# Kernel tuning notes

Measured on AMD Instinct MI355X. Metric: run time of the kernel, lower is better.

## Reference

```python
import jax, jax.numpy as jnp
import numpy as np

WS = 7
HEADS = 8
DIM = 256
IN_DIM = 128
HID = 1024
EPS = 1e-5


def _rel_index(ws):
    coords = np.stack(np.meshgrid(np.arange(ws), np.arange(ws), indexing='ij'))  # (2,ws,ws)
    cf = coords.reshape(2, -1)                      # (2,N)
    rel = (cf[:, :, None] - cf[:, None, :]).transpose(1, 2, 0).copy()  # (N,N,2)
    rel[..., 0] += ws - 1
    rel[..., 1] += ws - 1
    rel[..., 0] *= 2 * ws - 1
    return rel.sum(-1)  # (N,N) int

REL_IDX = jnp.asarray(_rel_index(WS).reshape(-1))


def layernorm(x, g, b):
    mu = jnp.mean(x, axis=-1, keepdims=True)
    var = jnp.mean(jnp.square(x - mu), axis=-1, keepdims=True)
    return (x - mu) * jax.lax.rsqrt(var + EPS) * g + b


def setup_inputs() -> dict:
    key = jax.random.key(0)
    ks = jax.random.split(key, 16)
    s = 0.02
    return {
        'x': jax.random.normal(ks[0], (16, IN_DIM, 56, 56), jnp.float32),
        'conv_w': jax.random.normal(ks[1], (DIM, IN_DIM, 3, 3), jnp.float32) * s,
        'conv_b': jnp.zeros((DIM,), jnp.float32),
        'g1': jnp.ones((DIM,), jnp.float32), 'b1': jnp.zeros((DIM,), jnp.float32),
        'g2': jnp.ones((DIM,), jnp.float32), 'b2': jnp.zeros((DIM,), jnp.float32),
        'g3': jnp.ones((DIM,), jnp.float32), 'b3': jnp.zeros((DIM,), jnp.float32),
        'qkv_w': jax.random.normal(ks[2], (3 * DIM, DIM), jnp.float32) * s,
        'rel_bias_table': jax.random.normal(ks[3], ((2 * WS - 1) ** 2, HEADS), jnp.float32) * s,
        'proj_w': jax.random.normal(ks[4], (DIM, DIM), jnp.float32) * s,
        'proj_b': jnp.zeros((DIM,), jnp.float32),
        'fc1_w': jax.random.normal(ks[5], (HID, DIM), jnp.float32) * s,
        'fc1_b': jnp.zeros((HID,), jnp.float32),
        'fc2_w': jax.random.normal(ks[6], (DIM, HID), jnp.float32) * s,
        'fc2_b': jnp.zeros((DIM,), jnp.float32),
    }


def reference(x, conv_w, conv_b, g1, b1, g2, b2, g3, b3, qkv_w, rel_bias_table,
              proj_w, proj_b, fc1_w, fc1_b, fc2_w, fc2_b):
    # proj_q: 3x3 conv, stride 1, pad 1 (input_dim != embed_dim)
    x = jax.lax.conv_general_dilated(
        x, conv_w, window_strides=(1, 1), padding=((1, 1), (1, 1)),
        dimension_numbers=('NCHW', 'OIHW', 'NCHW')) + conv_b[None, :, None, None]
    b, c, h, w = x.shape
    x = x.reshape(b, c, h * w).transpose(0, 2, 1)  # (b, n, c)
    x = layernorm(x, g1, b1)
    x = x.reshape(b, h, w, c)
    pb = (WS - h % WS) % WS
    pr = (WS - w % WS) % WS
    x = jnp.pad(x, ((0, 0), (0, pb), (0, pr), (0, 0)))
    hp, wp = h + pb, w + pr
    # window partition -> (nW, N, c)
    xw = x.reshape(b, hp // WS, WS, wp // WS, WS, c)
    xw = xw.transpose(0, 1, 3, 2, 4, 5).reshape(-1, WS * WS, c)
    nW, N, _ = xw.shape
    d = c // HEADS
    qkv = (xw @ qkv_w.T).reshape(nW, N, 3, HEADS, d).transpose(2, 0, 3, 1, 4)  # (3,nW,h,N,d)
    q, k, v = qkv[0] * (d ** -0.5), qkv[1], qkv[2]
    attn = jnp.einsum('whnd,whmd->whnm', q, k)
    bias = rel_bias_table[REL_IDX].reshape(N, N, HEADS).transpose(2, 0, 1)  # (h,N,N)
    attn = jax.nn.softmax(attn + bias[None], axis=-1)
    out = jnp.einsum('whnm,whmd->whnd', attn, v).transpose(0, 2, 1, 3).reshape(nW, N, c)
    out = out @ proj_w.T + proj_b
    # window reverse
    x = out.reshape(b, hp // WS, wp // WS, WS, WS, c)
    x = x.transpose(0, 1, 3, 2, 4, 5).reshape(b, hp, wp, c)
    x = x[:, :h, :w, :].reshape(b, h * w, c)
    # NOTE: faithful to source — NO residual from pre-attention stream
    x = layernorm(x, g2, b2)
    x = jax.nn.gelu(x @ fc1_w.T + fc1_b, approximate=False) @ fc2_w.T + fc2_b
    x = x + x  # source: x = x + drop_path(x) with identity drop_path
    x = layernorm(x, g3, b3)
    return x.reshape(b, h, w, c).transpose(0, 3, 1, 2)
```

## Files before the change

### kernel.cpp

```cpp
#include <hip/hip_runtime.h>
#include <hip/hip_bf16.h>

typedef unsigned short u16;
typedef unsigned int   u32;

#define TTOK  50176
#define CDIM  256

using short8 = __attribute__((ext_vector_type(8))) short;
using f32x4  = __attribute__((ext_vector_type(4))) float;

__device__ __forceinline__ float b2f(u16 u) { return __uint_as_float(((u32)u) << 16); }
__device__ __forceinline__ u16 f2b(float f) {
    u32 x = __float_as_uint(f);
    return (u16)((x + 0x7fffu + ((x >> 16) & 1u)) >> 16);
}

#define GLD16(src, dst) __builtin_amdgcn_global_load_lds( \
    (const __attribute__((address_space(1))) void*)(src),  \
    (__attribute__((address_space(3))) void*)(dst), 16, 0, 0)

__global__ __launch_bounds__(256) void cvt4_k(const float* __restrict__ a, const float* __restrict__ b,
                                              const float* __restrict__ c, const float* __restrict__ d,
                                              u16* __restrict__ dst) {
    int i = blockIdx.x * 256 + threadIdx.x;
    const float* src; int off;
    if (i < 49152)       { src = a; off = i; }
    else if (i < 65536)  { src = b; off = i - 49152; }
    else if (i < 131072) { src = c; off = i - 65536; }
    else                 { src = d; off = i - 131072; }
    float4 v = *(const float4*)&src[off * 4];
    ushort4 o;
    o.x = f2b(v.x); o.y = f2b(v.y); o.z = f2b(v.z); o.w = f2b(v.w);
    *(ushort4*)&dst[i * 4] = o;
}

__global__ __launch_bounds__(256) void pad_k(const float* __restrict__ x, u16* __restrict__ xp) {
    __shared__ float tile[128][58];
    int bid = blockIdx.x;
    int b = bid / 58, hp = bid - b * 58;
    int tid = threadIdx.x;
    bool zrow = (hp == 0 || hp == 57);
    if (!zrow) {
        int h = hp - 1;
        for (int e = tid; e < 128 * 14; e += 256) {
            int ic = e / 14, j = e - ic * 14;
            float4 v = *(const float4*)&x[(((size_t)b * 128 + ic) * 56 + h) * 56 + j * 4];
            tile[ic][j * 4 + 0] = v.x; tile[ic][j * 4 + 1] = v.y;
            tile[ic][j * 4 + 2] = v.z; tile[ic][j * 4 + 3] = v.w;
        }
        __syncthreads();
    }
    size_t rb = ((size_t)b * 58 + hp) * 58 * 128;
    for (int u = tid; u < 58 * 16; u += 256) {
        int wp = u / 16, icg = u - wp * 16;
        uint4 o = make_uint4(0u, 0u, 0u, 0u);
        if (!zrow && wp != 0 && wp != 57) {
            int w = wp - 1, ic0 = icg * 8;
            u16 v0 = f2b(tile[ic0 + 0][w]), v1 = f2b(tile[ic0 + 1][w]);
            u16 v2 = f2b(tile[ic0 + 2][w]), v3 = f2b(tile[ic0 + 3][w]);
            u16 v4 = f2b(tile[ic0 + 4][w]), v5 = f2b(tile[ic0 + 5][w]);
            u16 v6 = f2b(tile[ic0 + 6][w]), v7 = f2b(tile[ic0 + 7][w]);
            o.x = (u32)v0 | ((u32)v1 << 16);
            o.y = (u32)v2 | ((u32)v3 << 16);
            o.z = (u32)v4 | ((u32)v5 << 16);
            o.w = (u32)v6 | ((u32)v7 << 16);
        }
        *(uint4*)&xp[rb + (size_t)wp * 128 + icg * 8] = o;
    }
}

__global__ __launch_bounds__(256) void w2_k(const float* __restrict__ w, u16* __restrict__ o2) {
    int e = blockIdx.x * 256 + threadIdx.x;
    int o = e / 1152, rem = e - o * 1152;
    int tap = rem >> 7, ic = rem & 127;
    o2[e] = f2b(w[(o * 128 + ic) * 9 + tap]);
}

__device__ __forceinline__ void xcd_remap(int& bx, int& by) {
    int nx = gridDim.x, ny = gridDim.y;
    if ((ny & 7) == 0) {
        int linear = blockIdx.y * nx + blockIdx.x;
        int xcd = linear & 7, within = linear >> 3;
        bx = within % nx;
        by = xcd * (ny >> 3) + within / nx;
    } else { bx = blockIdx.x; by = blockIdx.y; }
}

__device__ __forceinline__ int xcd_remap1d() {
    int nb = gridDim.x, lin = blockIdx.x;
    int q = nb >> 3, r = nb & 7;
    int xcd = lin & 7, idx = lin >> 3;
    return (xcd < r ? xcd * (q + 1) : r * (q + 1) + (xcd - r) * q) + idx;
}

__global__ __launch_bounds__(256) void gemm_conv_ln_k(const u16* __restrict__ xp, const u16* __restrict__ W2,
                                                      const float* __restrict__ bias,
                                                      const float* __restrict__ gam, const float* __restrict__ bet,
                                                      u16* __restrict__ C) {
    __shared__ __align__(16) u16 lsA[64 * 64];
    __shared__ __align__(16) u16 lsB[256 * 64];
    int tid = threadIdx.x;
    int wave = tid >> 6, lane = tid & 63;
    int by = xcd_remap1d();
    int mBase = by * 64;
    int wm = wave >> 1, wn = wave & 1;
    int lr = lane & 15, lq = lane >> 4;
    int r8 = lane >> 3, kg = lane & 7;
    int kgsw = ((kg ^ r8) & 7) * 8;

    size_t tb[2]; const u16* gB[8];
#pragma unroll
    for (int j = 0; j < 2; ++j) {
        int t = mBase + wave * 16 + j * 8 + r8;
        int win = t / 49, n = t - win * 49;
        int b = win >> 6, wh = (win >> 3) & 7, ww = win & 7;
        int r = n / 7, s = n - r * 7;
        tb[j] = ((size_t)(b * 58 + wh * 7 + r) * 58 + ww * 7 + s) * 128 + kgsw;
    }
#pragma unroll
    for (int j = 0; j < 8; ++j)
        gB[j] = W2 + (size_t)(wave * 64 + j * 8 + r8) * 1152 + kgsw;

    f32x4 acc[2][8];
#pragma unroll
    for (int m = 0; m < 2; ++m)
#pragma unroll
        for (int n = 0; n < 8; ++n) acc[m][n] = (f32x4){0.f, 0.f, 0.f, 0.f};

    for (int ks = 0; ks < 18; ++ks) {
        int tap = ks >> 1, half = ks & 1;
        int kh = tap / 3, kw = tap - kh * 3;
        int uoff = (kh * 58 + kw) * 128 + half * 64;
#pragma unroll
        for (int j = 0; j < 2; ++j) GLD16(xp + tb[j] + uoff, lsA + (wave * 16 + j * 8) * 64);
#pragma unroll
        for (int j = 0; j < 8; ++j) GLD16(gB[j] + ks * 64, lsB + (wave * 64 + j * 8) * 64);
        __syncthreads();
#pragma unroll
        for (int kk = 0; kk < 2; ++kk) {
            int sl = (((kk << 2) | lq) ^ (lr & 7)) * 8;
            short8 af[2], bf[8];
#pragma unroll
            for (int m = 0; m < 2; ++m)
                af[m] = *(const short8*)&lsA[(wm * 32 + m * 16 + lr) * 64 + sl];
#pragma unroll
            for (int n = 0; n < 8; ++n)
                bf[n] = *(const short8*)&lsB[(wn * 128 + n * 16 + lr) * 64 + sl];
#pragma unroll
            for (int m = 0; m < 2; ++m)
#pragma unroll
                for (int n = 0; n < 8; ++n)
                    acc[m][n] = __builtin_amdgcn_mfma_f32_16x16x32_bf16(af[m], bf[n], acc[m][n], 0, 0, 0);
        }
        __syncthreads();
    }

    float bv[8], gv[8], btv[8];
#pragma unroll
    for (int n = 0; n < 8; ++n) {
        int col = wn * 128 + n * 16 + lr;
        bv[n] = bias[col]; gv[n] = gam[col]; btv[n] = bet[col];
    }
#pragma unroll
    for (int m = 0; m < 2; ++m)
#pragma unroll
        for (int n = 0; n < 8; ++n)
#pragma unroll
            for (int r = 0; r < 4; ++r) acc[m][n][r] += bv[n];

    float* red = (float*)lsA;
#pragma unroll
    for (int m = 0; m < 2; ++m)
#pragma unroll
        for (int r = 0; r < 4; ++r) {
            float s = 0.f, qq = 0.f;
#pragma unroll
            for (int n = 0; n < 8; ++n) { float v = acc[m][n][r]; s += v; qq += v * v; }
            s += __shfl_xor(s, 1); s += __shfl_xor(s, 2); s += __shfl_xor(s, 4); s += __shfl_xor(s, 8);
            qq += __shfl_xor(qq, 1); qq += __shfl_xor(qq, 2); qq += __shfl_xor(qq, 4); qq += __shfl_xor(qq, 8);
            if (lr == 0) {
                int row = wm * 32 + m * 16 + lq * 4 + r;
                red[row * 4 + wn * 2] = s; red[row * 4 + wn * 2 + 1] = qq;
            }
        }
    __syncthreads();

#pragma unroll
    for (int m = 0; m < 2; ++m)
#pragma unroll
        for (int r = 0; r < 4; ++r) {
            int row = wm * 32 + m * 16 + lq * 4 + r;
            float S = red[row * 4] + red[row * 4 + 2];
            float Q = red[row * 4 + 1] + red[row * 4 + 3];
            float mean = S * (1.f / 256.f);
            float var = Q * (1.f / 256.f) - mean * mean;
            float inv = rsqrtf(var + 1e-5f);
            size_t grow = (size_t)(mBase + row) * 256;
#pragma unroll
            for (int n = 0; n < 8; ++n) {
                int col = wn * 128 + n * 16 + lr;
                C[grow + col] = f2b((acc[m][n][r] - mean) * inv * gv[n] + btv[n]);
            }
        }
}

__global__ __launch_bounds__(256) void gemm_ln_k(const u16* __restrict__ A, const u16* __restrict__ Bw,
                                                 const float* __restrict__ bias,
                                                 const float* __restrict__ gam, const float* __restrict__ bet,
                                                 u16* __restrict__ C, int K) {
    __shared__ __align__(16) u16 lsA[64 * 64];
    __shared__ __align__(16) u16 lsB[256 * 64];
    int tid = threadIdx.x;
    int wave = tid >> 6, lane = tid & 63;
    int by = xcd_remap1d();
    int mBase = by * 64;
    int wm = wave >> 1, wn = wave & 1;
    int lr = lane & 15, lq = lane >> 4;
    int r8 = lane >> 3, kg = lane & 7;
    int kgsw = ((kg ^ r8) & 7) * 8;

    const u16* gA[2]; const u16* gB[8];
#pragma unroll
    for (int j = 0; j < 2; ++j)
        gA[j] = A + (size_t)(mBase + wave * 16 + j * 8 + r8) * K + kgsw;
#pragma unroll
    for (int j = 0; j < 8; ++j)
        gB[j] = Bw + (size_t)(wave * 64 + j * 8 + r8) * K + kgsw;

    f32x4 acc[2][8];
#pragma unroll
    for (int m = 0; m < 2; ++m)
#pragma unroll
        for (int n = 0; n < 8; ++n) acc[m][n] = (f32x4){0.f, 0.f, 0.f, 0.f};

    for (int k0 = 0; k0 < K; k0 += 64) {
#pragma unroll
        for (int j = 0; j < 2; ++j) GLD16(gA[j] + k0, lsA + (wave * 16 + j * 8) * 64);
#pragma unroll
        for (int j = 0; j < 8; ++j) GLD16(gB[j] + k0, lsB + (wave * 64 + j * 8) * 64);
        __syncthreads();
#pragma unroll
        for (int kk = 0; kk < 2; ++kk) {
            int sl = (((kk << 2) | lq) ^ (lr & 7)) * 8;
            short8 af[2], bf[8];
#pragma unroll
            for (int m = 0; m < 2; ++m)
                af[m] = *(const short8*)&lsA[(wm * 32 + m * 16 + lr) * 64 + sl];
#pragma unroll
            for (int n = 0; n < 8; ++n)
                bf[n] = *(const short8*)&lsB[(wn * 128 + n * 16 + lr) * 64 + sl];
#pragma unroll
            for (int m = 0; m < 2; ++m)
#pragma unroll
                for (int n = 0; n < 8; ++n)
                    acc[m][n] = __builtin_amdgcn_mfma_f32_16x16x32_bf16(af[m], bf[n], acc[m][n], 0, 0, 0);
        }
        __syncthreads();
    }

    float bv[8], gv[8], btv[8];
#pragma unroll
    for (int n = 0; n < 8; ++n) {
        int col = wn * 128 + n * 16 + lr;
        bv[n] = bias[col]; gv[n] = gam[col]; btv[n] = bet[col];
    }
#pragma unroll
    for (int m = 0; m < 2; ++m)
#pragma unroll
        for (int n = 0; n < 8; ++n)
#pragma unroll
            for (int r = 0; r < 4; ++r) acc[m][n][r] += bv[n];

    float* red = (float*)lsA;
#pragma unroll
    for (int m = 0; m < 2; ++m)
#pragma unroll
        for (int r = 0; r < 4; ++r) {
            float s = 0.f, qq = 0.f;
#pragma unroll
            for (int n = 0; n < 8; ++n) { float v = acc[m][n][r]; s += v; qq += v * v; }
            s += __shfl_xor(s, 1); s += __shfl_xor(s, 2); s += __shfl_xor(s, 4); s += __shfl_xor(s, 8);
            qq += __shfl_xor(qq, 1); qq += __shfl_xor(qq, 2); qq += __shfl_xor(qq, 4); qq += __shfl_xor(qq, 8);
            if (lr == 0) {
                int row = wm * 32 + m * 16 + lq * 4 + r;
                red[row * 4 + wn * 2] = s; red[row * 4 + wn * 2 + 1] = qq;
            }
        }
    __syncthreads();

#pragma unroll
    for (int m = 0; m < 2; ++m)
#pragma unroll
        for (int r = 0; r < 4; ++r) {
            int row = wm * 32 + m * 16 + lq * 4 + r;
            float S = red[row * 4] + red[row * 4 + 2];
            float Q = red[row * 4 + 1] + red[row * 4 + 3];
            float mean = S * (1.f / 256.f);
            float var = Q * (1.f / 256.f) - mean * mean;
            float inv = rsqrtf(var + 1e-5f);
            size_t grow = (size_t)(mBase + row) * 256;
#pragma unroll
            for (int n = 0; n < 8; ++n) {
                int col = wn * 128 + n * 16 + lr;
                C[grow + col] = f2b((acc[m][n][r] - mean) * inv * gv[n] + btv[n]);
            }
        }
}

template <int EPI>
__global__ __launch_bounds__(256) void gemm_k(const u16* __restrict__ A, const u16* __restrict__ Bw,
                                              const float* __restrict__ bias, u16* __restrict__ C,
                                              int M, int N, int K) {
    __shared__ __align__(16) u16 lsA[2][128 * 32];
    __shared__ __align__(16) u16 lsB[2][128 * 32];
    int tid = threadIdx.x;
    int wave = tid >> 6, lane = tid & 63;
    int bx, by; xcd_remap(bx, by);
    int mBase = by * 128, nBase = bx * 128;
    int wm = wave >> 1, wn = wave & 1;
    int lr = lane & 15, lq = lane >> 4;
    int rr = lane >> 2, kc = lane & 3;
    int kcs = (kc ^ ((rr >> 1) & 3)) * 8;

    const u16* gA[2]; const u16* gB[2];
#pragma unroll
    for (int j = 0; j < 2; ++j) {
        int row = wave * 32 + j * 16 + rr;
        gA[j] = A  + (size_t)(mBase + row) * K + kcs;
        gB[j] = Bw + (size_t)(nBase + row) * K + kcs;
    }

    f32x4 acc[4][4];
#pragma unroll
    for (int m = 0; m < 4; ++m)
#pragma unroll
        for (int n = 0; n < 4; ++n) acc[m][n] = (f32x4){0.f, 0.f, 0.f, 0.f};

    int nk = K >> 5;
#pragma unroll
    for (int j = 0; j < 2; ++j) {
        GLD16(gA[j], &lsA[0][(wave * 32 + j * 16) * 32]);
        GLD16(gB[j], &lsB[0][(wave * 32 + j * 16) * 32]);
    }
    __syncthreads();

    int slq = (lq ^ ((lr >> 1) & 3)) * 8;
    for (int ks = 0; ks < nk; ++ks) {
        int cur = ks & 1;
        if (ks + 1 < nk) {
            int nxt = cur ^ 1;
            int ko = (ks + 1) << 5;
#pragma unroll
            for (int j = 0; j < 2; ++j) {
                GLD16(gA[j] + ko, &lsA[nxt][(wave * 32 + j * 16) * 32]);
                GLD16(gB[j] + ko, &lsB[nxt][(wave * 32 + j * 16) * 32]);
            }
        }
        short8 af[4], bf[4];
#pragma unroll
        for (int m = 0; m < 4; ++m)
            af[m] = *(const short8*)&lsA[cur][(wm * 64 + m * 16 + lr) * 32 + slq];
#pragma unroll
        for (int n = 0; n < 4; ++n)
            bf[n] = *(const short8*)&lsB[cur][(wn * 64 + n * 16 + lr) * 32 + slq];
#pragma unroll
        for (int m = 0; m < 4; ++m)
#pragma unroll
            for (int n = 0; n < 4; ++n)
                acc[m][n] = __builtin_amdgcn_mfma_f32_16x16x32_bf16(af[m], bf[n], acc[m][n], 0, 0, 0);
        __syncthreads();
    }

#pragma unroll
    for (int m = 0; m < 4; ++m) {
        int row0 = mBase + wm * 64 + m * 16 + lq * 4;
#pragma unroll
        for (int n = 0; n < 4; ++n) {
            int col = nBase + wn * 64 + n * 16 + lr;
            float bv = (EPI >= 1) ? bias[col] : 0.f;
#pragma unroll
            for (int r = 0; r < 4; ++r) {
                float v = acc[m][n][r] + bv;
                if (EPI == 2) {
                    float u = 0.79788456f * (v + 0.044715f * v * v * v);
                    float e = __expf(-2.f * u);
                    v = v * __frcp_rn(1.f + e);
                }
                C[(size_t)(row0 + r) * N + col] = f2b(v);
            }
        }
    }
}

__global__ __launch_bounds__(256) void attn_mfma_k(const u16* __restrict__ qkv,
                                                   const float* __restrict__ tab,
                                                   u16* __restrict__ out) {
    __shared__ __align__(16) u16 sh[28488];
    int tid = threadIdx.x;
    int wave = tid >> 6, lane = tid & 63;
    int wh = blockIdx.x * 4 + wave;
    int win = wh >> 3, head = wh & 7;
    int g = lane >> 4, cc = lane & 15;

    u16* Pl = sh + wave * 4608;
    u16* Vl = sh + 18432 + wave * 2176;
    float* bs = (float*)(sh + 27136) + wave * 169;

    const size_t wbase = (size_t)win * 49 * 768;
    for (int e = lane; e < 169; e += 64) bs[e] = tab[e * 8 + head];
    for (int e = lane; e < 49 * 16; e += 64) {
        int k = e >> 4, d0 = (e & 15) * 2;
        *(u32*)&Vl[k * 34 + d0] = *(const u32*)&qkv[wbase + (size_t)k * 768 + 512 + head * 32 + d0];
    }
    for (int e = lane; e < 15 * 16; e += 64) {
        int k = 49 + (e >> 4), d0 = (e & 15) * 2;
        *(u32*)&Vl[k * 34 + d0] = 0u;
    }
    __syncthreads();

    short8 aQ[4], bK[4];
#pragma unroll
    for (int t = 0; t < 4; ++t) {
        int qr = t * 16 + cc; if (qr > 48) qr = 48;
        aQ[t] = *(const short8*)&qkv[wbase + (size_t)qr * 768 + head * 32 + g * 8];
        int kr = t * 16 + cc; if (kr > 48) kr = 48;
        bK[t] = *(const short8*)&qkv[wbase + (size_t)kr * 768 + 256 + head * 32 + g * 8];
    }
    f32x4 S[4][4];
#pragma unroll
    for (int a = 0; a < 4; ++a)
#pragma unroll
        for (int b = 0; b < 4; ++b)
            S[a][b] = __builtin_amdgcn_mfma_f32_16x16x32_bf16(aQ[a], bK[b], (f32x4){0.f,0.f,0.f,0.f}, 0, 0, 0);

    int AqA[4][4];
#pragma unroll
    for (int tr = 0; tr < 4; ++tr)
#pragma unroll
        for (int r = 0; r < 4; ++r) {
            int q = tr * 16 + g * 4 + r; if (q > 48) q = 48;
            int dq = (q * 37) >> 8;
            AqA[tr][r] = 6 * dq + q + 84;
        }
    int AcA[4];
    bool colBad[4];
#pragma unroll
    for (int tc = 0; tc < 4; ++tc) {
        int c = tc * 16 + cc;
        colBad[tc] = (c > 48);
        if (c > 48) c = 48;
        int dc = (c * 37) >> 8;
        AcA[tc] = 6 * dc + c;
    }
    const float scale = 0.17677669529663687f;
    float inv[4][4];
#pragma unroll
    for (int tr = 0; tr < 4; ++tr) {
#pragma unroll
        for (int r = 0; r < 4; ++r) {
            float z0 = colBad[0] ? -1e30f : S[tr][0][r] * scale + bs[AqA[tr][r] - AcA[0]];
            float z1 = colBad[1] ? -1e30f : S[tr][1][r] * scale + bs[AqA[tr][r] - AcA[1]];
            float z2 = colBad[2] ? -1e30f : S[tr][2][r] * scale + bs[AqA[tr][r] - AcA[2]];
            float z3 = colBad[3] ? -1e30f : S[tr][3][r] * scale + bs[AqA[tr][r] - AcA[3]];
            float mx = fmaxf(fmaxf(z0, z1), fmaxf(z2, z3));
            mx = fmaxf(mx, __shfl_xor(mx, 1));
            mx = fmaxf(mx, __shfl_xor(mx, 2));
            mx = fmaxf(mx, __shfl_xor(mx, 4));
            mx = fmaxf(mx, __shfl_xor(mx, 8));
            float p0 = __expf(z0 - mx), p1 = __expf(z1 - mx);
            float p2 = __expf(z2 - mx), p3 = __expf(z3 - mx);
            S[tr][0][r] = p0; S[tr][1][r] = p1; S[tr][2][r] = p2; S[tr][3][r] = p3;
            float sm = p0 + p1 + p2 + p3;
            sm += __shfl_xor(sm, 1); sm += __shfl_xor(sm, 2);
            sm += __shfl_xor(sm, 4); sm += __shfl_xor(sm, 8);
            inv[tr][r] = 1.0f / sm;
        }
    }

#pragma unroll
    for (int tr = 0; tr < 4; ++tr)
#pragma unroll
        for (int tc = 0; tc < 4; ++tc) {
            int k = tc * 16 + cc;
            u16* pb = &Pl[tr * 1152 + k * 18 + g * 4];
            u32 w0 = (u32)f2b(S[tr][tc][0]) | ((u32)f2b(S[tr][tc][1]) << 16);
            u32 w1 = (u32)f2b(S[tr][tc][2]) | ((u32)f2b(S[tr][tc][3]) << 16);
            *(u32*)pb = w0;
            *(u32*)(pb + 2) = w1;
        }
    __syncthreads();

    f32x4 O[4][2];
#pragma unroll
    for (int a = 0; a < 4; ++a) { O[a][0] = (f32x4){0.f,0.f,0.f,0.f}; O[a][1] = (f32x4){0.f,0.f,0.f,0.f}; }
#pragma unroll
    for (int s = 0; s < 2; ++s) {
        short8 pa[4], vb[2];
#pragma unroll
        for (int tr = 0; tr < 4; ++tr)
#pragma unroll
            for (int j = 0; j < 8; ++j)
                pa[tr][j] = (short)Pl[tr * 1152 + (s * 32 + g * 8 + j) * 18 + cc];
#pragma unroll
        for (int td = 0; td < 2; ++td)
#pragma unroll
            for (int j = 0; j < 8; ++j)
                vb[td][j] = (short)Vl[(s * 32 + g * 8 + j) * 34 + td * 16 + cc];
#pragma unroll
        for (int tr = 0; tr < 4; ++tr)
#pragma unroll
            for (int td = 0; td < 2; ++td)
                O[tr][td] = __builtin_amdgcn_mfma_f32_16x16x32_bf16(pa[tr], vb[td], O[tr][td], 0, 0, 0);
    }

#pragma unroll
    for (int tr = 0; tr < 4; ++tr)
#pragma unroll
        for (int r = 0; r < 4; ++r) {
            int q = tr * 16 + g * 4 + r;
            if (q < 49) {
                float iv = inv[tr][r];
                u16* op = out + (size_t)(win * 49 + q) * 256 + head * 32;
                op[cc]      = f2b(O[tr][0][r] * iv);
                op[16 + cc] = f2b(O[tr][1][r] * iv);
            }
        }
}

__global__ __launch_bounds__(256) void ln3_out_k(const u16* __restrict__ f, const float* __restrict__ g3,
                                                 const float* __restrict__ b3, float* __restrict__ out) {
    __shared__ float tile[256][57];
    int bh = blockIdx.x;
    int b = bh / 56, h = bh - b * 56;
    int wv = threadIdx.x >> 6, lane = threadIdx.x & 63;
    int wh = h / 7, r = h - wh * 7;
    float4 gg = *(const float4*)&g3[lane * 4];
    float4 bb = *(const float4*)&b3[lane * 4];
    for (int i = 0; i < 14; ++i) {
        int w = wv + i * 4;
        int wwn = w / 7, s2 = w - wwn * 7;
        int t = (b * 64 + wh * 8 + wwn) * 49 + r * 7 + s2;
        ushort4 u = *(const ushort4*)&f[(size_t)t * 256 + lane * 4];
        float v0 = 2.f * b2f(u.x), v1 = 2.f * b2f(u.y), v2 = 2.f * b2f(u.z), v3 = 2.f * b2f(u.w);
        float s = v0 + v1 + v2 + v3;
        float q = v0 * v0 + v1 * v1 + v2 * v2 + v3 * v3;
#pragma unroll
        for (int o = 32; o; o >>= 1) { s += __shfl_xor(s, o); q += __shfl_xor(q, o); }
        float mean = s * (1.f / 256.f);
        float var = q * (1.f / 256.f) - mean * mean;
        float inv = rsqrtf(var + 1e-5f);
        int c = lane * 4;
        tile[c + 0][w] = (v0 - mean) * inv * gg.x + bb.x;
        tile[c + 1][w] = (v1 - mean) * inv * gg.y + bb.y;
        tile[c + 2][w] = (v2 - mean) * inv * gg.z + bb.z;
        tile[c + 3][w] = (v3 - mean) * inv * gg.w + bb.w;
    }
    __syncthreads();
    size_t obase = (size_t)b * 256 * 3136 + (size_t)h * 56;
#pragma unroll
    for (int it = 0; it < 28; ++it) {
        int e = it * 256 + threadIdx.x;
        int c = e / 28, wu = e - c * 28;
        float2 pack = make_float2(tile[c][wu * 2], tile[c][wu * 2 + 1]);
        *(float2*)&out[obase + (size_t)c * 3136 + wu * 2] = pack;
    }
}

extern "C" void kernel_launch(void* const* d_in, const int* in_sizes, int n_in,
                              void* d_out, int out_size, void* d_ws, size_t ws_size,
                              hipStream_t stream) {
    (void)in_sizes; (void)n_in; (void)out_size;
    const float* x      = (const float*)d_in[0];
    const float* conv_w = (const float*)d_in[1];
    const float* conv_b = (const float*)d_in[2];
    const float* g1     = (const float*)d_in[3];
    const float* b1     = (const float*)d_in[4];
    const float* g2     = (const float*)d_in[5];
    const float* b2     = (const float*)d_in[6];
    const float* g3     = (const float*)d_in[7];
    const float* b3     = (const float*)d_in[8];
    const float* qkv_w  = (const float*)d_in[9];
    const float* tab    = (const float*)d_in[10];
    const float* proj_w = (const float*)d_in[11];
    const float* proj_b = (const float*)d_in[12];
    const float* fc1_w  = (const float*)d_in[13];
    const float* fc1_b  = (const float*)d_in[14];
    const float* fc2_w  = (const float*)d_in[15];
    const float* fc2_b  = (const float*)d_in[16];
    float* outp = (float*)d_out;

    const size_t OFF_Y  = (size_t)TTOK * 1152 * 2;
    const size_t OFF_AT = OFF_Y + (size_t)TTOK * 512;
    const size_t NEED   = OFF_AT + (size_t)TTOK * 512;
    if (ws_size < NEED) return;

    char* ws = (char*)d_ws;
    u16* xpad    = (u16*)ws;
    u16* ybuf    = (u16*)(ws + OFF_Y);
    u16* atout   = (u16*)(ws + OFF_AT);
    u16* qkvbuf  = (u16*)ws;
    u16* hidden  = (u16*)ws;
    u16* W2      = atout;
    u16* wbase   = (u16*)(ws + (size_t)TTOK * 1024 * 2);
    u16* qkvw_b  = wbase;
    u16* projw_b = wbase + 196608;
    u16* fc1w_b  = projw_b + 65536;
    u16* fc2w_b  = fc1w_b + 262144;

    pad_k<<<928, 256, 0, stream>>>(x, xpad);
    w2_k<<<1152, 256, 0, stream>>>(conv_w, W2);
    cvt4_k<<<768, 256, 0, stream>>>(qkv_w, proj_w, fc1_w, fc2_w, qkvw_b);
    gemm_conv_ln_k<<<784, 256, 0, stream>>>(xpad, W2, conv_b, g1, b1, ybuf);
    gemm_k<0><<<dim3(6, 392), 256, 0, stream>>>(ybuf, qkvw_b, nullptr, qkvbuf, TTOK, 768, 256);
    attn_mfma_k<<<2048, 256, 0, stream>>>(qkvbuf, tab, atout);
    gemm_ln_k<<<784, 256, 0, stream>>>(atout, projw_b, proj_b, g2, b2, ybuf, 256);
    gemm_k<2><<<dim3(8, 392), 256, 0, stream>>>(ybuf, fc1w_b, fc1_b, hidden, TTOK, 1024, 256);
    gemm_k<1><<<dim3(2, 392), 256, 0, stream>>>(hidden, fc2w_b, fc2_b, atout, TTOK, 256, 1024);
    ln3_out_k<<<896, 256, 0, stream>>>(atout, g3, b3, outp);
}
```

Before: 326.1 us.

## Double-buffer LDS in conv/LN GEMMs and vectorize general GEMM epilogue stores

```diff
diff --git a/kernel.cpp b/kernel.cpp
--- a/kernel.cpp
+++ b/kernel.cpp
@@ -98,29 +98,29 @@
                                                       const float* __restrict__ bias,
                                                       const float* __restrict__ gam, const float* __restrict__ bet,
                                                       u16* __restrict__ C) {
-    __shared__ __align__(16) u16 lsA[64 * 64];
-    __shared__ __align__(16) u16 lsB[256 * 64];
+    __shared__ __align__(16) u16 lsA[2][64 * 32];
+    __shared__ __align__(16) u16 lsB[2][256 * 32];
     int tid = threadIdx.x;
     int wave = tid >> 6, lane = tid & 63;
     int by = xcd_remap1d();
     int mBase = by * 64;
     int wm = wave >> 1, wn = wave & 1;
     int lr = lane & 15, lq = lane >> 4;
-    int r8 = lane >> 3, kg = lane & 7;
-    int kgsw = ((kg ^ r8) & 7) * 8;
-
-    size_t tb[2]; const u16* gB[8];
-#pragma unroll
-    for (int j = 0; j < 2; ++j) {
-        int t = mBase + wave * 16 + j * 8 + r8;
+    int rr4 = lane >> 2, kc = lane & 3;
+    int kcs = (kc ^ ((rr4 >> 1) & 3)) * 8;
+
+    size_t tbA;
+    {
+        int t = mBase + wave * 16 + rr4;
         int win = t / 49, n = t - win * 49;
         int b = win >> 6, wh = (win >> 3) & 7, ww = win & 7;
         int r = n / 7, s = n - r * 7;
-        tb[j] = ((size_t)(b * 58 + wh * 7 + r) * 58 + ww * 7 + s) * 128 + kgsw;
-    }
-#pragma unroll
-    for (int j = 0; j < 8; ++j)
-        gB[j] = W2 + (size_t)(wave * 64 + j * 8 + r8) * 1152 + kgsw;
+        tbA = ((size_t)(b * 58 + wh * 7 + r) * 58 + ww * 7 + s) * 128 + kcs;
+    }
+    const u16* gB[4];
+#pragma unroll
+    for (int j = 0; j < 4; ++j)
+        gB[j] = W2 + (size_t)(j * 64 + wave * 16 + rr4) * 1152 + kcs;
 
     f32x4 acc[2][8];
 #pragma unroll
@@ -128,33 +128,36 @@
 #pragma unroll
         for (int n = 0; n < 8; ++n) acc[m][n] = (f32x4){0.f, 0.f, 0.f, 0.f};
 
-    for (int ks = 0; ks < 18; ++ks) {
-        int tap = ks >> 1, half = ks & 1;
-        int kh = tap / 3, kw = tap - kh * 3;
-        int uoff = (kh * 58 + kw) * 128 + half * 64;
-#pragma unroll
-        for (int j = 0; j < 2; ++j) GLD16(xp + tb[j] + uoff, lsA + (wave * 16 + j * 8) * 64);
-#pragma unroll
-        for (int j = 0; j < 8; ++j) GLD16(gB[j] + ks * 64, lsB + (wave * 64 + j * 8) * 64);
+#define CONV_STAGE(ks, buf) do { \
+        int tap_ = (ks) >> 2, qz_ = (ks) & 3; \
+        int kh_ = tap_ / 3, kw_ = tap_ - kh_ * 3; \
+        GLD16(xp + tbA + (kh_ * 58 + kw_) * 128 + qz_ * 32, &lsA[buf][(wave * 16 + rr4) * 32]); \
+        _Pragma("unroll") \
+        for (int j_ = 0; j_ < 4; ++j_) \
+            GLD16(gB[j_] + (ks) * 32, &lsB[buf][(j_ * 64 + wave * 16 + rr4) * 32]); \
+    } while (0)
+
+    CONV_STAGE(0, 0);
+    __syncthreads();
+    int slq = (lq ^ ((lr >> 1) & 3)) * 8;
+    for (int ks = 0; ks < 36; ++ks) {
+        int cur = ks & 1;
+        if (ks + 1 < 36) CONV_STAGE(ks + 1, cur ^ 1);
+        short8 af[2], bf[8];
+#pragma unroll
+        for (int m = 0; m < 2; ++m)
+            af[m] = *(const short8*)&lsA[cur][(wm * 32 + m * 16 + lr) * 32 + slq];
+#pragma unroll
+        for (int n = 0; n < 8; ++n)
+            bf[n] = *(const short8*)&lsB[cur][(wn * 128 + n * 16 + lr) * 32 + slq];
+#pragma unroll
+        for (int m = 0; m < 2; ++m)
+#pragma unroll
+            for (int n = 0; n < 8; ++n)
+                acc[m][n] = __builtin_amdgcn_mfma_f32_16x16x32_bf16(af[m], bf[n], acc[m][n], 0, 0, 0);
         __syncthreads();
-#pragma unroll
-        for (int kk = 0; kk < 2; ++kk) {
-            int sl = (((kk << 2) | lq) ^ (lr & 7)) * 8;
-            short8 af[2], bf[8];
-#pragma unroll
-            for (int m = 0; m < 2; ++m)
-                af[m] = *(const short8*)&lsA[(wm * 32 + m * 16 + lr) * 64 + sl];
-#pragma unroll
-            for (int n = 0; n < 8; ++n)
-                bf[n] = *(const short8*)&lsB[(wn * 128 + n * 16 + lr) * 64 + sl];
-#pragma unroll
-            for (int m = 0; m < 2; ++m)
-#pragma unroll
-                for (int n = 0; n < 8; ++n)
-                    acc[m][n] = __builtin_amdgcn_mfma_f32_16x16x32_bf16(af[m], bf[n], acc[m][n], 0, 0, 0);
-        }
-        __syncthreads();
-    }
+    }
+#undef CONV_STAGE
 
     float bv[8], gv[8], btv[8];
 #pragma unroll
@@ -209,24 +212,22 @@
                                                  const float* __restrict__ bias,
                                                  const float* __restrict__ gam, const float* __restrict__ bet,
                                                  u16* __restrict__ C, int K) {
-    __shared__ __align__(16) u16 lsA[64 * 64];
-    __shared__ __align__(16) u16 lsB[256 * 64];
+    __shared__ __align__(16) u16 lsA[2][64 * 32];
+    __shared__ __align__(16) u16 lsB[2][256 * 32];
     int tid = threadIdx.x;
     int wave = tid >> 6, lane = tid & 63;
     int by = xcd_remap1d();
     int mBase = by * 64;
     int wm = wave >> 1, wn = wave & 1;
     int lr = lane & 15, lq = lane >> 4;
-    int r8 = lane >> 3, kg = lane & 7;
-    int kgsw = ((kg ^ r8) & 7) * 8;
-
-    const u16* gA[2]; const u16* gB[8];
-#pragma unroll
-    for (int j = 0; j < 2; ++j)
-        gA[j] = A + (size_t)(mBase + wave * 16 + j * 8 + r8) * K + kgsw;
-#pragma unroll
-    for (int j = 0; j < 8; ++j)
-        gB[j] = Bw + (size_t)(wave * 64 + j * 8 + r8) * K + kgsw;
+    int rr4 = lane >> 2, kc = lane & 3;
+    int kcs = (kc ^ ((rr4 >> 1) & 3)) * 8;
+
+    const u16* gA = A + (size_t)(mBase + wave * 16 + rr4) * K + kcs;
+    const u16* gB[4];
+#pragma unroll
+    for (int j = 0; j < 4; ++j)
+        gB[j] = Bw + (size_t)(j * 64 + wave * 16 + rr4) * K + kcs;
 
     f32x4 acc[2][8];
 #pragma unroll
@@ -234,30 +235,35 @@
 #pragma unroll
         for (int n = 0; n < 8; ++n) acc[m][n] = (f32x4){0.f, 0.f, 0.f, 0.f};
 
-    for (int k0 = 0; k0 < K; k0 += 64) {
-#pragma unroll
-        for (int j = 0; j < 2; ++j) GLD16(gA[j] + k0, lsA + (wave * 16 + j * 8) * 64);
-#pragma unroll
-        for (int j = 0; j < 8; ++j) GLD16(gB[j] + k0, lsB + (wave * 64 + j * 8) * 64);
+#define LN_STAGE(ks, buf) do { \
+        GLD16(gA + (ks) * 32, &lsA[buf][(wave * 16 + rr4) * 32]); \
+        _Pragma("unroll") \
+        for (int j_ = 0; j_ < 4; ++j_) \
+            GLD16(gB[j_] + (ks) * 32, &lsB[buf][(j_ * 64 + wave * 16 + rr4) * 32]); \
+    } while (0)
+
+    int nk = K >> 5;
+    LN_STAGE(0, 0);
+    __syncthreads();
+    int slq = (lq ^ ((lr >> 1) & 3)) * 8;
+    for (int ks = 0; ks < nk; ++ks) {
+        int cur = ks & 1;
+        if (ks + 1 < nk) LN_STAGE(ks + 1, cur ^ 1);
+        short8 af[2], bf[8];
+#pragma unroll
+        for (int m = 0; m < 2; ++m)
+            af[m] = *(const short8*)&lsA[cur][(wm * 32 + m * 16 + lr) * 32 + slq];
+#pragma unroll
+        for (int n = 0; n < 8; ++n)
+            bf[n] = *(const short8*)&lsB[cur][(wn * 128 + n * 16 + lr) * 32 + slq];
+#pragma unroll
+        for (int m = 0; m < 2; ++m)
+#pragma unroll
+            for (int n = 0; n < 8; ++n)
+                acc[m][n] = __builtin_amdgcn_mfma_f32_16x16x32_bf16(af[m], bf[n], acc[m][n], 0, 0, 0);
         __syncthreads();
-#pragma unroll
-        for (int kk = 0; kk < 2; ++kk) {
-            int sl = (((kk << 2) | lq) ^ (lr & 7)) * 8;
-            short8 af[2], bf[8];
-#pragma unroll
-            for (int m = 0; m < 2; ++m)
-                af[m] = *(const short8*)&lsA[(wm * 32 + m * 16 + lr) * 64 + sl];
-#pragma unroll
-            for (int n = 0; n < 8; ++n)
-                bf[n] = *(const short8*)&lsB[(wn * 128 + n * 16 + lr) * 64 + sl];
-#pragma unroll
-            for (int m = 0; m < 2; ++m)
-#pragma unroll
-                for (int n = 0; n < 8; ++n)
-                    acc[m][n] = __builtin_amdgcn_mfma_f32_16x16x32_bf16(af[m], bf[n], acc[m][n], 0, 0, 0);
-        }
-        __syncthreads();
-    }
+    }
+#undef LN_STAGE
 
     float bv[8], gv[8], btv[8];
 #pragma unroll
@@ -368,27 +374,37 @@
         for (int m = 0; m < 4; ++m)
 #pragma unroll
             for (int n = 0; n < 4; ++n)
-                acc[m][n] = __builtin_amdgcn_mfma_f32_16x16x32_bf16(af[m], bf[n], acc[m][n], 0, 0, 0);
+                acc[m][n] = __builtin_amdgcn_mfma_f32_16x16x32_bf16(bf[n], af[m], acc[m][n], 0, 0, 0);
         __syncthreads();
     }
 
 #pragma unroll
     for (int m = 0; m < 4; ++m) {
-        int row0 = mBase + wm * 64 + m * 16 + lq * 4;
+        int row = mBase + wm * 64 + m * 16 + lr;
+        u16* crow = C + (size_t)row * N;
 #pragma unroll
         for (int n = 0; n < 4; ++n) {
-            int col = nBase + wn * 64 + n * 16 + lr;
-            float bv = (EPI >= 1) ? bias[col] : 0.f;
-#pragma unroll
-            for (int r = 0; r < 4; ++r) {
-                float v = acc[m][n][r] + bv;
-                if (EPI == 2) {
-                    float u = 0.79788456f * (v + 0.044715f * v * v * v);
-                    float e = __expf(-2.f * u);
-                    v = v * __frcp_rn(1.f + e);
-                }
-                C[(size_t)(row0 + r) * N + col] = f2b(v);
-            }
+            int col0 = nBase + wn * 64 + n * 16 + lq * 4;
+            float b0 = 0.f, b1 = 0.f, b2 = 0.f, b3 = 0.f;
+            if (EPI >= 1) {
+                float4 bv4 = *(const float4*)&bias[col0];
+                b0 = bv4.x; b1 = bv4.y; b2 = bv4.z; b3 = bv4.w;
+            }
+            float v0 = acc[m][n][0] + b0, v1 = acc[m][n][1] + b1;
+            float v2 = acc[m][n][2] + b2, v3 = acc[m][n][3] + b3;
+            if (EPI == 2) {
+                float u0 = 0.79788456f * (v0 + 0.044715f * v0 * v0 * v0);
+                float u1 = 0.79788456f * (v1 + 0.044715f * v1 * v1 * v1);
+                float u2 = 0.79788456f * (v2 + 0.044715f * v2 * v2 * v2);
+                float u3 = 0.79788456f * (v3 + 0.044715f * v3 * v3 * v3);
+                v0 = v0 * __frcp_rn(1.f + __expf(-2.f * u0));
+                v1 = v1 * __frcp_rn(1.f + __expf(-2.f * u1));
+                v2 = v2 * __frcp_rn(1.f + __expf(-2.f * u2));
+                v3 = v3 * __frcp_rn(1.f + __expf(-2.f * u3));
+            }
+            ushort4 o;
+            o.x = f2b(v0); o.y = f2b(v1); o.z = f2b(v2); o.w = f2b(v3);
+            *(ushort4*)&crow[col0] = o;
         }
     }
 }
```

New measurement: 373.0 us. 14.4% more time.
